# Kernel tuning notes

Hardware: AMD Instinct MI355X
Metric: run time of the kernel (lower is better)

The kernel has to match this reference:

```python
import jax, jax.numpy as jnp
import numpy as np

B, T, C = 1, 4096, 1024
NH, NKV, HD = 16, 4, 64
N_REP = NH // NKV
WIN = 1024
EPS = 1e-5
ROPE_THETA = 10000.0


def setup_inputs() -> dict:
    key = jax.random.key(0)
    ks = jax.random.split(key, 6)
    s = 1.0 / np.sqrt(C)
    x = jax.random.normal(ks[0], (B, T, C), jnp.float32)
    wq = jax.random.normal(ks[1], (NH * HD, C), jnp.float32) * s
    wk = jax.random.normal(ks[2], (NKV * HD, C), jnp.float32) * s
    wv = jax.random.normal(ks[3], (NKV * HD, C), jnp.float32) * s
    wo = jax.random.normal(ks[4], (C, NH * HD), jnp.float32) * (1.0 / np.sqrt(NH * HD))
    q_norm_w = jnp.ones((HD,), jnp.float32)
    k_norm_w = jnp.ones((HD,), jnp.float32)
    # RoPE tables: (T, HD//2)
    inv_freq = 1.0 / (ROPE_THETA ** (np.arange(0, HD, 2, dtype=np.float32) / HD))
    ang = np.outer(np.arange(T, dtype=np.float32), inv_freq)
    freqs_cos = jnp.asarray(np.cos(ang), jnp.float32)
    freqs_sin = jnp.asarray(np.sin(ang), jnp.float32)
    return {"x": x, "wq": wq, "wk": wk, "wv": wv, "wo": wo,
            "q_norm_w": q_norm_w, "k_norm_w": k_norm_w,
            "freqs_cos": freqs_cos, "freqs_sin": freqs_sin}


def _rmsnorm(v, w):
    # RMSNorm over last dim (per-head)
    return v * jax.lax.rsqrt(jnp.mean(v * v, axis=-1, keepdims=True) + EPS) * w


def _rope(v, cos, sin):
    # v: (B, T, H, HD); interleaved complex rotation, matching torch polar freqs_cis
    vr, vi = v[..., 0::2], v[..., 1::2]
    c = cos[None, :, None, :]
    s = sin[None, :, None, :]
    out_r = vr * c - vi * s
    out_i = vr * s + vi * c
    return jnp.stack([out_r, out_i], axis=-1).reshape(v.shape)


def reference(x, wq, wk, wv, wo, q_norm_w, k_norm_w, freqs_cos, freqs_sin):
    xq = jnp.einsum('btc,dc->btd', x, wq).reshape(B, T, NH, HD)
    xk = jnp.einsum('btc,dc->btd', x, wk).reshape(B, T, NKV, HD)
    xv = jnp.einsum('btc,dc->btd', x, wv).reshape(B, T, NKV, HD)
    # per-head QK RMSNorm
    xq = _rmsnorm(xq, q_norm_w)
    xk = _rmsnorm(xk, k_norm_w)
    # RoPE
    xq = _rope(xq, freqs_cos, freqs_sin)
    xk = _rope(xk, freqs_cos, freqs_sin)
    # GQA: expand kv heads
    xk = jnp.repeat(xk, N_REP, axis=2)  # (B, T, NH, HD)
    xv = jnp.repeat(xv, N_REP, axis=2)
    scale = 1.0 / np.sqrt(HD)
    scores = jnp.einsum('bthd,bshd->bhts', xq, xk) * scale
    i = jnp.arange(T)[:, None]
    j = jnp.arange(T)[None, :]
    mask = (i >= j) & (i - j < WIN)  # causal + sliding window
    scores = jnp.where(mask[None, None], scores, -jnp.inf)
    attn = jax.nn.softmax(scores, axis=-1)
    y = jnp.einsum('bhts,bshd->bthd', attn, xv).reshape(B, T, NH * HD)
    return jnp.einsum('btd,cd->btc', y, wo)
```

## Files before the change

kernel.cpp:

```cpp
#include <hip/hip_runtime.h>
#include <hip/hip_bf16.h>


#define WIN_SZ 1024

typedef __attribute__((ext_vector_type(8))) short short8;
typedef __attribute__((ext_vector_type(8))) unsigned short ushort8;
typedef __attribute__((ext_vector_type(4))) float f32x4;
typedef __attribute__((ext_vector_type(16))) float f32x16;

#define GLOAD_LDS16(g, s)                                              \
  __builtin_amdgcn_global_load_lds(                                    \
      (const __attribute__((address_space(1))) unsigned int*)(g),      \
      (__attribute__((address_space(3))) unsigned int*)(s), 16, 0, 0)

__device__ __forceinline__ unsigned short f2bf(float f) {
  union { float f; unsigned u; } v; v.f = f;
  unsigned r = v.u + 0x7fffu + ((v.u >> 16) & 1u);
  return (unsigned short)(r >> 16);
}

__device__ __forceinline__ float bf2f(unsigned short b) {
  union { unsigned u; float f; } v; v.u = ((unsigned)b) << 16; return v.f;
}

__device__ __forceinline__ unsigned pk2bf(float lo, float hi) {
  __hip_bfloat162 h = __float22bfloat162_rn(make_float2(lo, hi));
  union { __hip_bfloat162 h; unsigned u; } c; c.h = h; return c.u;
}

__device__ __forceinline__ short8 frag4(unsigned w0, unsigned w1, unsigned w2, unsigned w3) {
  union { unsigned u[4]; short8 s; } x;
  x.u[0] = w0; x.u[1] = w1; x.u[2] = w2; x.u[3] = w3; return x.s;
}

__global__ __launch_bounds__(256) void k_f2b_all(const float* __restrict__ x,
                                                 const float* __restrict__ wq,
                                                 const float* __restrict__ wk,
                                                 const float* __restrict__ wv,
                                                 const float* __restrict__ wo,
                                                 unsigned short* __restrict__ xb,
                                                 unsigned short* __restrict__ wqkvb,
                                                 unsigned short* __restrict__ wob) {
  int q = blockIdx.x * 256 + threadIdx.x;
  const float* src;
  unsigned short* dst;
  int off;
  if (q < 1048576) { src = x; dst = xb; off = q; }
  else if (q < 1310720) { src = wq; dst = wqkvb; off = q - 1048576; }
  else if (q < 1376256) { src = wk; dst = wqkvb + 1024 * 1024; off = q - 1310720; }
  else if (q < 1441792) { src = wv; dst = wqkvb + 1280 * 1024; off = q - 1376256; }
  else { src = wo; dst = wob; off = q - 1441792; }
  float4 v = ((const float4*)src)[off];
  ushort4 o;
  o.x = f2bf(v.x); o.y = f2bf(v.y); o.z = f2bf(v.z); o.w = f2bf(v.w);
  ((ushort4*)dst)[off] = o;
}

template <int BF16OUT>
__global__ __launch_bounds__(256) void k_gemm2p(const unsigned short* __restrict__ A,
                                                const unsigned short* __restrict__ B,
                                                void* __restrict__ Cv,
                                                int M, int N, int K) {
  __shared__ unsigned short As[2][128 * 64];
  __shared__ unsigned short Bs[2][128 * 64];
  const int tid = threadIdx.x;
  const int w = tid >> 6, l = tid & 63;
  const int wr = w >> 1, wc = w & 1;
  const int r = l & 15, g = l >> 4;
  const int m0 = blockIdx.y * 128, n0 = blockIdx.x * 128;
  const int lr = l >> 3, lc = l & 7;
  const int srowb = w * 32;

  f32x4 acc[4][4];
#pragma unroll
  for (int i = 0; i < 4; i++)
#pragma unroll
    for (int j = 0; j < 4; j++) acc[i][j] = {0.f, 0.f, 0.f, 0.f};

  const unsigned short* Ag = A + (size_t)(m0 + srowb + lr) * K + lc * 8;
  const unsigned short* Bg = B + (size_t)(n0 + srowb + lr) * K + lc * 8;

  auto stage = [&](int buf, int k0) {
#pragma unroll
    for (int it = 0; it < 4; it++) {
      GLOAD_LDS16(Ag + (size_t)(it * 8) * K + k0, &As[buf][(srowb + it * 8) * 64]);
      GLOAD_LDS16(Bg + (size_t)(it * 8) * K + k0, &Bs[buf][(srowb + it * 8) * 64]);
    }
  };

  stage(0, 0);
  __syncthreads();
  int cur = 0;
  const int NT = K >> 6;
  for (int t = 0; t < NT; ++t) {
    if (t + 1 < NT) stage(cur ^ 1, (t + 1) << 6);
    const char* Ab = (const char*)As[cur];
    const char* Bb = (const char*)Bs[cur];
#pragma unroll
    for (int kk = 0; kk < 2; kk++) {
      short8 af[4], bfr[4];
#pragma unroll
      for (int mi = 0; mi < 4; mi++)
        af[mi] = *(const short8*)(Ab + (wr * 64 + mi * 16 + r) * 128 + kk * 64 + g * 16);
#pragma unroll
      for (int nj = 0; nj < 4; nj++)
        bfr[nj] = *(const short8*)(Bb + (wc * 64 + nj * 16 + r) * 128 + kk * 64 + g * 16);
#pragma unroll
      for (int mi = 0; mi < 4; mi++)
#pragma unroll
        for (int nj = 0; nj < 4; nj++)
          acc[mi][nj] = __builtin_amdgcn_mfma_f32_16x16x32_bf16(af[mi], bfr[nj], acc[mi][nj], 0, 0, 0);
    }
    __syncthreads();
    cur ^= 1;
  }

#pragma unroll
  for (int mi = 0; mi < 4; mi++)
#pragma unroll
    for (int nj = 0; nj < 4; nj++) {
      int row = m0 + wr * 64 + mi * 16 + g * 4;
      int col = n0 + wc * 64 + nj * 16 + r;
      if (BF16OUT) {
        unsigned short* C = (unsigned short*)Cv;
#pragma unroll
        for (int e = 0; e < 4; e++)
          C[(size_t)(row + e) * N + col] = f2bf(acc[mi][nj][e]);
      } else {
        float* C = (float*)Cv;
#pragma unroll
        for (int e = 0; e < 4; e++)
          C[(size_t)(row + e) * N + col] = acc[mi][nj][e];
      }
    }
}

__global__ __launch_bounds__(256) void k_normrope(const unsigned short* __restrict__ QKV,
                                                  const float* __restrict__ qw,
                                                  const float* __restrict__ kw,
                                                  const float* __restrict__ fc,
                                                  const float* __restrict__ fs,
                                                  unsigned short* __restrict__ Qb,
                                                  unsigned short* __restrict__ Kb,
                                                  unsigned short* __restrict__ Vtg) {
  int gid = blockIdx.x * 4 + (threadIdx.x >> 6);
  int l = threadIdx.x & 63;
  int t = gid / 24;
  int u = gid - t * 24;
  if (u < 16) {
    float v = bf2f(QKV[(size_t)t * 1536 + u * 64 + l]);
    float ss = v * v;
#pragma unroll
    for (int off = 32; off; off >>= 1) ss += __shfl_xor(ss, off);
    float rms = rsqrtf(ss * (1.0f / 64.0f) + 1e-5f);
    float vn = v * rms * qw[l];
    float c = fc[t * 32 + (l >> 1)], s = fs[t * 32 + (l >> 1)];
    float p = __shfl_xor(vn, 1);
    float out = (l & 1) ? (p * s + vn * c) : (vn * c - p * s);
    Qb[(size_t)t * 1024 + u * 64 + l] = f2bf(out * 0.1803368801111204f);
  } else if (u < 20) {
    int hh = u - 16;
    float v = bf2f(QKV[(size_t)t * 1536 + 1024 + hh * 64 + l]);
    float ss = v * v;
#pragma unroll
    for (int off = 32; off; off >>= 1) ss += __shfl_xor(ss, off);
    float rms = rsqrtf(ss * (1.0f / 64.0f) + 1e-5f);
    float vn = v * rms * kw[l];
    float c = fc[t * 32 + (l >> 1)], s = fs[t * 32 + (l >> 1)];
    float p = __shfl_xor(vn, 1);
    float out = (l & 1) ? (p * s + vn * c) : (vn * c - p * s);
    Kb[(size_t)t * 256 + hh * 64 + l] = f2bf(out);
  } else {
    int hh = u - 20;
    Vtg[(size_t)(hh * 64 + l) * 4096 + t] = QKV[(size_t)t * 1536 + 1280 + hh * 64 + l];
  }
}

__global__ __launch_bounds__(512, 4) void k_attn4(const unsigned short* __restrict__ Qb,
                                                  const unsigned short* __restrict__ Kb,
                                                  const unsigned short* __restrict__ Vtg,
                                                  unsigned short* __restrict__ Yb) {
  __shared__ char smem[4 * 8192 + 1024];
  char* stage = smem;
  float* Obuf = (float*)smem;
  float* ml = (float*)(smem + 32768);

  const int id = blockIdx.x;
  const int cupair = id & 255, sel = id >> 8;
  int qi = cupair >> 1;
  if (sel) qi = 127 - qi;
  const int hk = (cupair & 1) * 2 + sel;
  const int q0 = qi * 32;

  const int tid = threadIdx.x, w = tid >> 6, l = tid & 63;
  const int hh = w & 3, half = w >> 2;
  const int h = hk * 4 + hh;
  const int l31 = l & 31, hi = l >> 5, l15 = l & 15;
  const int qrow = q0 + l31;

  int jlo = q0 - (WIN_SZ - 1);
  if (jlo < 0) jlo = 0;
  jlo &= ~63;
  const int jlast = ((q0 + 31) >> 6) << 6;
  const int nt = ((jlast - jlo) >> 6) + 1;
  const int nh0 = (nt + 1) >> 1;

  const int sb = tid >> 7;
  const int su = tid & 127;
  const int srow = su >> 1;
  const int sg = (su & 1) * 4;
  const int sbase = sb * 8192 + (srow & 31) * 256;
  const int srx = (srow & 15) << 4;
  const int srh = (srow >> 5) * 128;
  const bool isV = sb & 1;
  const unsigned short* gK = Kb + (size_t)srow * 256 + hk * 64 + sg * 8;
  const unsigned short* gV = Vtg + (size_t)(hk * 64 + srow) * 4096 + sg * 8;

  short8 qf[4];
#pragma unroll
  for (int ks = 0; ks < 4; ks++)
    qf[ks] = *(const short8*)(Qb + (size_t)qrow * 1024 + h * 64 + ks * 16 + hi * 8);

  f32x16 accO0, accO1;
#pragma unroll
  for (int i = 0; i < 16; i++) { accO0[i] = 0.f; accO1[i] = 0.f; }
  float m = -1e30f, lsum = 0.f;

  ushort8 pre[4];
  auto prefetch = [&](int s) {
    int jt0 = jlo + (s << 6);
    int t1 = nh0 + s;
    int jt1 = (t1 < nt) ? (jlo + (t1 << 6)) : jlo;
    int jt = (sb >= 2) ? jt1 : jt0;
    if (!isV) {
      const unsigned short* g = gK + (size_t)jt * 256;
#pragma unroll
      for (int e = 0; e < 4; e++) pre[e] = *(const ushort8*)(g + e * 8);
    } else {
      const unsigned short* g = gV + jt;
#pragma unroll
      for (int e = 0; e < 4; e++) pre[e] = *(const ushort8*)(g + e * 8);
    }
  };
  prefetch(0);

  const int kbase = half * 16384;
  const int vbase = kbase + 8192;

  for (int s = 0; s < nh0; ++s) {
    __syncthreads();
#pragma unroll
    for (int e = 0; e < 4; e++) {
      int dst = sbase + ((srh + (sg + e) * 16) ^ srx);
      *(ushort8*)(stage + dst) = pre[e];
    }
    __syncthreads();
    if (s + 1 < nh0) prefetch(s + 1);

    const int myt = half ? (nh0 + s) : s;
    if (myt < nt) {
      const int jt = jlo + (myt << 6);

      f32x16 st0, st1;
#pragma unroll
      for (int i = 0; i < 16; i++) { st0[i] = 0.f; st1[i] = 0.f; }
      __builtin_amdgcn_s_setprio(1);
#pragma unroll
      for (int ks = 0; ks < 4; ks++) {
        int colb = ks * 32 + hi * 16;
        short8 kf0 = *(const short8*)(stage + kbase + l31 * 256 + (colb ^ (l15 << 4)));
        st0 = __builtin_amdgcn_mfma_f32_32x32x16_bf16(kf0, qf[ks], st0, 0, 0, 0);
        short8 kf1 = *(const short8*)(stage + kbase + l31 * 256 + ((128 + colb) ^ (l15 << 4)));
        st1 = __builtin_amdgcn_mfma_f32_32x32x16_bf16(kf1, qf[ks], st1, 0, 0, 0);
      }
      __builtin_amdgcn_s_setprio(0);

      if (jt + 63 > q0 || (q0 + 31) - jt >= WIN_SZ) {
        const int jb = jt + hi * 4;
#pragma unroll
        for (int rg = 0; rg < 16; rg++) {
          int j0 = jb + (rg & 3) + 8 * (rg >> 2);
          if (!((j0 <= qrow) && (qrow - j0 < WIN_SZ))) st0[rg] = -3.0e38f;
          int j1 = j0 + 32;
          if (!((j1 <= qrow) && (qrow - j1 < WIN_SZ))) st1[rg] = -3.0e38f;
        }
      }

      float mx = st0[0];
#pragma unroll
      for (int rg = 1; rg < 16; rg++) mx = fmaxf(mx, st0[rg]);
#pragma unroll
      for (int rg = 0; rg < 16; rg++) mx = fmaxf(mx, st1[rg]);
      mx = fmaxf(mx, __shfl_xor(mx, 32));
      if (!__all(mx <= m + 8.0f)) {
        float mnew = fmaxf(m, mx);
        float alpha = exp2f(m - mnew);
#pragma unroll
        for (int rg = 0; rg < 16; rg++) { accO0[rg] *= alpha; accO1[rg] *= alpha; }
        lsum *= alpha;
        m = mnew;
      }
      float ps = 0.f;
#pragma unroll
      for (int rg = 0; rg < 16; rg++) { st0[rg] = exp2f(st0[rg] - m); ps += st0[rg]; }
#pragma unroll
      for (int rg = 0; rg < 16; rg++) { st1[rg] = exp2f(st1[rg] - m); ps += st1[rg]; }
      lsum += ps;

      unsigned pd0[2][4], pd1[2][4];
#pragma unroll
      for (int b = 0; b < 4; b++) {
        pd0[0][b] = pk2bf(st0[4 * b], st0[4 * b + 1]);
        pd1[0][b] = pk2bf(st0[4 * b + 2], st0[4 * b + 3]);
        pd0[1][b] = pk2bf(st1[4 * b], st1[4 * b + 1]);
        pd1[1][b] = pk2bf(st1[4 * b + 2], st1[4 * b + 3]);
      }

      __builtin_amdgcn_s_setprio(1);
#pragma unroll
      for (int jj = 0; jj < 2; jj++) {
#pragma unroll
        for (int ks2 = 0; ks2 < 2; ks2++) {
          unsigned a0 = pd0[jj][2 * ks2], a1 = pd0[jj][2 * ks2 + 1];
          unsigned b0 = pd1[jj][2 * ks2], b1 = pd1[jj][2 * ks2 + 1];
          unsigned a0x = __shfl_xor(a0, 32), a1x = __shfl_xor(a1, 32);
          unsigned b0x = __shfl_xor(b0, 32), b1x = __shfl_xor(b1, 32);
          unsigned w0 = hi ? a1x : a0;
          unsigned w1 = hi ? b1x : b0;
          unsigned w2 = hi ? a1 : a0x;
          unsigned w3 = hi ? b1 : b0x;
          short8 pf = frag4(w0, w1, w2, w3);
          int colb2 = jj * 64 + ks2 * 32 + hi * 16;
          short8 vf0 = *(const short8*)(stage + vbase + l31 * 256 + (colb2 ^ (l15 << 4)));
          accO0 = __builtin_amdgcn_mfma_f32_32x32x16_bf16(vf0, pf, accO0, 0, 0, 0);
          short8 vf1 = *(const short8*)(stage + vbase + l31 * 256 + ((128 + colb2) ^ (l15 << 4)));
          accO1 = __builtin_amdgcn_mfma_f32_32x32x16_bf16(vf1, pf, accO1, 0, 0, 0);
        }
      }
      __builtin_amdgcn_s_setprio(0);
    }
  }

  lsum += __shfl_xor(lsum, 32);
  __syncthreads();
  if (half == 1) {
#pragma unroll
    for (int dd = 0; dd < 2; dd++) {
      const f32x16& a = dd ? accO1 : accO0;
#pragma unroll
      for (int rg = 0; rg < 16; rg++) {
        int d = dd * 32 + 8 * (rg >> 2) + 4 * hi + (rg & 3);
        Obuf[(hh * 64 + d) * 32 + l31] = a[rg];
      }
    }
    if (!hi) { ml[(hh * 2 + 0) * 32 + l31] = m; ml[(hh * 2 + 1) * 32 + l31] = lsum; }
  }
  __syncthreads();
  if (half == 0) {
    float m1 = ml[(hh * 2 + 0) * 32 + l31];
    float l1 = ml[(hh * 2 + 1) * 32 + l31];
    float ms = fmaxf(m, m1);
    float a0 = exp2f(m - ms), a1 = exp2f(m1 - ms);
    float inv = 1.0f / (lsum * a0 + l1 * a1);
    a0 *= inv; a1 *= inv;
#pragma unroll
    for (int dd = 0; dd < 2; dd++) {
      const f32x16& a = dd ? accO1 : accO0;
#pragma unroll
      for (int b = 0; b < 4; b++) {
        float o[4];
#pragma unroll
        for (int e = 0; e < 4; e++) {
          int d = dd * 32 + 8 * b + 4 * hi + e;
          o[e] = a[4 * b + e] * a0 + Obuf[(hh * 64 + d) * 32 + l31] * a1;
        }
        union { unsigned u[2]; ushort4 v; } ov;
        ov.u[0] = pk2bf(o[0], o[1]);
        ov.u[1] = pk2bf(o[2], o[3]);
        *(ushort4*)(Yb + (size_t)qrow * 1024 + h * 64 + dd * 32 + b * 8 + hi * 4) = ov.v;
      }
    }
  }
}

extern "C" void kernel_launch(void* const* d_in, const int* in_sizes, int n_in,
                              void* d_out, int out_size, void* d_ws, size_t ws_size,
                              hipStream_t stream) {
  const float* x = (const float*)d_in[0];
  const float* wq = (const float*)d_in[1];
  const float* wk = (const float*)d_in[2];
  const float* wv = (const float*)d_in[3];
  const float* wo = (const float*)d_in[4];
  const float* qw = (const float*)d_in[5];
  const float* kw = (const float*)d_in[6];
  const float* fc = (const float*)d_in[7];
  const float* fs = (const float*)d_in[8];
  float* out = (float*)d_out;

  char* p = (char*)d_ws;
  auto alloc = [&](size_t b) {
    char* q = p;
    p += (b + 255) & ~(size_t)255;
    return q;
  };
  unsigned short* xb = (unsigned short*)alloc((size_t)4096 * 1024 * 2);
  unsigned short* wqkvb = (unsigned short*)alloc((size_t)1536 * 1024 * 2);
  unsigned short* wob = (unsigned short*)alloc((size_t)1024 * 1024 * 2);
  unsigned short* QKVb = (unsigned short*)alloc((size_t)4096 * 1536 * 2);
  unsigned short* Qb = (unsigned short*)alloc((size_t)4096 * 1024 * 2);
  unsigned short* Kb = (unsigned short*)alloc((size_t)4096 * 256 * 2);
  unsigned short* Vtg = (unsigned short*)alloc((size_t)256 * 4096 * 2);
  unsigned short* Yb = (unsigned short*)alloc((size_t)4096 * 1024 * 2);

  k_f2b_all<<<6656, 256, 0, stream>>>(x, wq, wk, wv, wo, xb, wqkvb, wob);
  k_gemm2p<1><<<dim3(12, 32), 256, 0, stream>>>(xb, wqkvb, QKVb, 4096, 1536, 1024);
  k_normrope<<<24576, 256, 0, stream>>>(QKVb, qw, kw, fc, fs, Qb, Kb, Vtg);
  k_attn4<<<512, 512, 0, stream>>>(Qb, Kb, Vtg, Yb);
  k_gemm2p<0><<<dim3(8, 32), 256, 0, stream>>>(Yb, wob, out, 4096, 1024, 1024);
}
```

Measured before the change: 123.2 us.

## Use persistent atomic work queue for attention and narrower swizzled GEMM tiles

Attention becomes a persistent kernel of 384 blocks. The blocks pull (query tile, kv head) units from a global atomic counter, ordered longest-first, which should balance the uneven sliding-window workload. The counter is reset by the norm/rope kernel. Both GEMMs switch to 128x64 tiles with a 1D grid and an XCD-aware block swizzle, doubling block count for better CU fill and L2 locality, at the cost of lower arithmetic intensity per block.

```diff
diff --git a/kernel.cpp b/kernel.cpp
--- a/kernel.cpp
+++ b/kernel.cpp
@@ -58,35 +58,41 @@
 }
 
 template <int BF16OUT>
-__global__ __launch_bounds__(256) void k_gemm2p(const unsigned short* __restrict__ A,
-                                                const unsigned short* __restrict__ B,
-                                                void* __restrict__ Cv,
-                                                int M, int N, int K) {
+__global__ __launch_bounds__(256) void k_gemmN64(const unsigned short* __restrict__ A,
+                                                 const unsigned short* __restrict__ B,
+                                                 void* __restrict__ Cv,
+                                                 int M, int N, int K, int nblk) {
   __shared__ unsigned short As[2][128 * 64];
-  __shared__ unsigned short Bs[2][128 * 64];
+  __shared__ unsigned short Bs[2][64 * 64];
+  const int id = blockIdx.x;
+  const int chunk = gridDim.x >> 3;
+  const int swz = (id & 7) * chunk + (id >> 3);
+  const int n_idx = swz % nblk, m_idx = swz / nblk;
+  const int m0 = m_idx * 128, n0 = n_idx * 64;
+
   const int tid = threadIdx.x;
   const int w = tid >> 6, l = tid & 63;
   const int wr = w >> 1, wc = w & 1;
   const int r = l & 15, g = l >> 4;
-  const int m0 = blockIdx.y * 128, n0 = blockIdx.x * 128;
   const int lr = l >> 3, lc = l & 7;
-  const int srowb = w * 32;
-
-  f32x4 acc[4][4];
+  const int srowb = w * 32, browb = w * 16;
+
+  f32x4 acc[4][2];
 #pragma unroll
   for (int i = 0; i < 4; i++)
 #pragma unroll
-    for (int j = 0; j < 4; j++) acc[i][j] = {0.f, 0.f, 0.f, 0.f};
+    for (int j = 0; j < 2; j++) acc[i][j] = {0.f, 0.f, 0.f, 0.f};
 
   const unsigned short* Ag = A + (size_t)(m0 + srowb + lr) * K + lc * 8;
-  const unsigned short* Bg = B + (size_t)(n0 + srowb + lr) * K + lc * 8;
+  const unsigned short* Bg = B + (size_t)(n0 + browb + lr) * K + lc * 8;
 
   auto stage = [&](int buf, int k0) {
 #pragma unroll
-    for (int it = 0; it < 4; it++) {
+    for (int it = 0; it < 4; it++)
       GLOAD_LDS16(Ag + (size_t)(it * 8) * K + k0, &As[buf][(srowb + it * 8) * 64]);
-      GLOAD_LDS16(Bg + (size_t)(it * 8) * K + k0, &Bs[buf][(srowb + it * 8) * 64]);
-    }
+#pragma unroll
+    for (int it = 0; it < 2; it++)
+      GLOAD_LDS16(Bg + (size_t)(it * 8) * K + k0, &Bs[buf][(browb + it * 8) * 64]);
   };
 
   stage(0, 0);
@@ -99,17 +105,17 @@
     const char* Bb = (const char*)Bs[cur];
 #pragma unroll
     for (int kk = 0; kk < 2; kk++) {
-      short8 af[4], bfr[4];
+      short8 af[4], bfr[2];
 #pragma unroll
       for (int mi = 0; mi < 4; mi++)
         af[mi] = *(const short8*)(Ab + (wr * 64 + mi * 16 + r) * 128 + kk * 64 + g * 16);
 #pragma unroll
-      for (int nj = 0; nj < 4; nj++)
-        bfr[nj] = *(const short8*)(Bb + (wc * 64 + nj * 16 + r) * 128 + kk * 64 + g * 16);
+      for (int nj = 0; nj < 2; nj++)
+        bfr[nj] = *(const short8*)(Bb + (wc * 32 + nj * 16 + r) * 128 + kk * 64 + g * 16);
 #pragma unroll
       for (int mi = 0; mi < 4; mi++)
 #pragma unroll
-        for (int nj = 0; nj < 4; nj++)
+        for (int nj = 0; nj < 2; nj++)
           acc[mi][nj] = __builtin_amdgcn_mfma_f32_16x16x32_bf16(af[mi], bfr[nj], acc[mi][nj], 0, 0, 0);
     }
     __syncthreads();
@@ -119,9 +125,9 @@
 #pragma unroll
   for (int mi = 0; mi < 4; mi++)
 #pragma unroll
-    for (int nj = 0; nj < 4; nj++) {
+    for (int nj = 0; nj < 2; nj++) {
       int row = m0 + wr * 64 + mi * 16 + g * 4;
-      int col = n0 + wc * 64 + nj * 16 + r;
+      int col = n0 + wc * 32 + nj * 16 + r;
       if (BF16OUT) {
         unsigned short* C = (unsigned short*)Cv;
 #pragma unroll
@@ -143,7 +149,9 @@
                                                   const float* __restrict__ fs,
                                                   unsigned short* __restrict__ Qb,
                                                   unsigned short* __restrict__ Kb,
-                                                  unsigned short* __restrict__ Vtg) {
+                                                  unsigned short* __restrict__ Vtg,
+                                                  int* __restrict__ ctr) {
+  if (blockIdx.x == 0 && threadIdx.x == 0) *ctr = 0;
   int gid = blockIdx.x * 4 + (threadIdx.x >> 6);
   int l = threadIdx.x & 63;
   int t = gid / 24;
@@ -177,34 +185,20 @@
   }
 }
 
-__global__ __launch_bounds__(512, 4) void k_attn4(const unsigned short* __restrict__ Qb,
+__global__ __launch_bounds__(512, 4) void k_attn5(const unsigned short* __restrict__ Qb,
                                                   const unsigned short* __restrict__ Kb,
                                                   const unsigned short* __restrict__ Vtg,
-                                                  unsigned short* __restrict__ Yb) {
+                                                  unsigned short* __restrict__ Yb,
+                                                  int* __restrict__ ctr) {
   __shared__ char smem[4 * 8192 + 1024];
+  __shared__ int s_unit;
   char* stage = smem;
   float* Obuf = (float*)smem;
   float* ml = (float*)(smem + 32768);
 
-  const int id = blockIdx.x;
-  const int cupair = id & 255, sel = id >> 8;
-  int qi = cupair >> 1;
-  if (sel) qi = 127 - qi;
-  const int hk = (cupair & 1) * 2 + sel;
-  const int q0 = qi * 32;
-
   const int tid = threadIdx.x, w = tid >> 6, l = tid & 63;
   const int hh = w & 3, half = w >> 2;
-  const int h = hk * 4 + hh;
   const int l31 = l & 31, hi = l >> 5, l15 = l & 15;
-  const int qrow = q0 + l31;
-
-  int jlo = q0 - (WIN_SZ - 1);
-  if (jlo < 0) jlo = 0;
-  jlo &= ~63;
-  const int jlast = ((q0 + 31) >> 6) << 6;
-  const int nt = ((jlast - jlo) >> 6) + 1;
-  const int nh0 = (nt + 1) >> 1;
 
   const int sb = tid >> 7;
   const int su = tid & 127;
@@ -214,171 +208,191 @@
   const int srx = (srow & 15) << 4;
   const int srh = (srow >> 5) * 128;
   const bool isV = sb & 1;
-  const unsigned short* gK = Kb + (size_t)srow * 256 + hk * 64 + sg * 8;
-  const unsigned short* gV = Vtg + (size_t)(hk * 64 + srow) * 4096 + sg * 8;
-
-  short8 qf[4];
-#pragma unroll
-  for (int ks = 0; ks < 4; ks++)
-    qf[ks] = *(const short8*)(Qb + (size_t)qrow * 1024 + h * 64 + ks * 16 + hi * 8);
-
-  f32x16 accO0, accO1;
-#pragma unroll
-  for (int i = 0; i < 16; i++) { accO0[i] = 0.f; accO1[i] = 0.f; }
-  float m = -1e30f, lsum = 0.f;
-
-  ushort8 pre[4];
-  auto prefetch = [&](int s) {
-    int jt0 = jlo + (s << 6);
-    int t1 = nh0 + s;
-    int jt1 = (t1 < nt) ? (jlo + (t1 << 6)) : jlo;
-    int jt = (sb >= 2) ? jt1 : jt0;
-    if (!isV) {
-      const unsigned short* g = gK + (size_t)jt * 256;
-#pragma unroll
-      for (int e = 0; e < 4; e++) pre[e] = *(const ushort8*)(g + e * 8);
-    } else {
-      const unsigned short* g = gV + jt;
-#pragma unroll
-      for (int e = 0; e < 4; e++) pre[e] = *(const ushort8*)(g + e * 8);
-    }
-  };
-  prefetch(0);
-
   const int kbase = half * 16384;
   const int vbase = kbase + 8192;
 
-  for (int s = 0; s < nh0; ++s) {
+  for (;;) {
     __syncthreads();
-#pragma unroll
-    for (int e = 0; e < 4; e++) {
-      int dst = sbase + ((srh + (sg + e) * 16) ^ srx);
-      *(ushort8*)(stage + dst) = pre[e];
+    if (tid == 0) s_unit = atomicAdd(ctr, 1);
+    __syncthreads();
+    const int u = s_unit;
+    if (u >= 512) break;
+    const int qi = 127 - (u >> 2);
+    const int hk = u & 3;
+    const int q0 = qi * 32;
+    const int h = hk * 4 + hh;
+    const int qrow = q0 + l31;
+
+    int jlo = q0 - (WIN_SZ - 1);
+    if (jlo < 0) jlo = 0;
+    jlo &= ~63;
+    const int jlast = ((q0 + 31) >> 6) << 6;
+    const int nt = ((jlast - jlo) >> 6) + 1;
+    const int nh0 = (nt + 1) >> 1;
+
+    const unsigned short* gK = Kb + (size_t)srow * 256 + hk * 64 + sg * 8;
+    const unsigned short* gV = Vtg + (size_t)(hk * 64 + srow) * 4096 + sg * 8;
+
+    short8 qf[4];
+#pragma unroll
+    for (int ks = 0; ks < 4; ks++)
+      qf[ks] = *(const short8*)(Qb + (size_t)qrow * 1024 + h * 64 + ks * 16 + hi * 8);
+
+    f32x16 accO0, accO1;
+#pragma unroll
+    for (int i = 0; i < 16; i++) { accO0[i] = 0.f; accO1[i] = 0.f; }
+    float m = -1e30f, lsum = 0.f;
+
+    ushort8 pre[4];
+    auto prefetch = [&](int s) {
+      int jt0 = jlo + (s << 6);
+      int t1 = nh0 + s;
+      int jt1 = (t1 < nt) ? (jlo + (t1 << 6)) : jlo;
+      int jt = (sb >= 2) ? jt1 : jt0;
+      if (!isV) {
+        const unsigned short* g = gK + (size_t)jt * 256;
+#pragma unroll
+        for (int e = 0; e < 4; e++) pre[e] = *(const ushort8*)(g + e * 8);
+      } else {
+        const unsigned short* g = gV + jt;
+#pragma unroll
+        for (int e = 0; e < 4; e++) pre[e] = *(const ushort8*)(g + e * 8);
+      }
+    };
+    prefetch(0);
+
+    for (int s = 0; s < nh0; ++s) {
+      __syncthreads();
+#pragma unroll
+      for (int e = 0; e < 4; e++) {
+        int dst = sbase + ((srh + (sg + e) * 16) ^ srx);
+        *(ushort8*)(stage + dst) = pre[e];
+      }
+      __syncthreads();
+      if (s + 1 < nh0) prefetch(s + 1);
+
+      const int myt = half ? (nh0 + s) : s;
+      if (myt < nt) {
+        const int jt = jlo + (myt << 6);
+
+        f32x16 st0, st1;
+#pragma unroll
+        for (int i = 0; i < 16; i++) { st0[i] = 0.f; st1[i] = 0.f; }
+        __builtin_amdgcn_s_setprio(1);
+#pragma unroll
+        for (int ks = 0; ks < 4; ks++) {
+          int colb = ks * 32 + hi * 16;
+          short8 kf0 = *(const short8*)(stage + kbase + l31 * 256 + (colb ^ (l15 << 4)));
+          st0 = __builtin_amdgcn_mfma_f32_32x32x16_bf16(kf0, qf[ks], st0, 0, 0, 0);
+          short8 kf1 = *(const short8*)(stage + kbase + l31 * 256 + ((128 + colb) ^ (l15 << 4)));
+          st1 = __builtin_amdgcn_mfma_f32_32x32x16_bf16(kf1, qf[ks], st1, 0, 0, 0);
+        }
+        __builtin_amdgcn_s_setprio(0);
+
+        if (jt + 63 > q0 || (q0 + 31) - jt >= WIN_SZ) {
+          const int jb = jt + hi * 4;
+#pragma unroll
+          for (int rg = 0; rg < 16; rg++) {
+            int j0 = jb + (rg & 3) + 8 * (rg >> 2);
+            if (!((j0 <= qrow) && (qrow - j0 < WIN_SZ))) st0[rg] = -3.0e38f;
+            int j1 = j0 + 32;
+            if (!((j1 <= qrow) && (qrow - j1 < WIN_SZ))) st1[rg] = -3.0e38f;
+          }
+        }
+
+        float mx = st0[0];
+#pragma unroll
+        for (int rg = 1; rg < 16; rg++) mx = fmaxf(mx, st0[rg]);
+#pragma unroll
+        for (int rg = 0; rg < 16; rg++) mx = fmaxf(mx, st1[rg]);
+        mx = fmaxf(mx, __shfl_xor(mx, 32));
+        if (!__all(mx <= m + 8.0f)) {
+          float mnew = fmaxf(m, mx);
+          float alpha = exp2f(m - mnew);
+#pragma unroll
+          for (int rg = 0; rg < 16; rg++) { accO0[rg] *= alpha; accO1[rg] *= alpha; }
+          lsum *= alpha;
+          m = mnew;
+        }
+        float ps = 0.f;
+#pragma unroll
+        for (int rg = 0; rg < 16; rg++) { st0[rg] = exp2f(st0[rg] - m); ps += st0[rg]; }
+#pragma unroll
+        for (int rg = 0; rg < 16; rg++) { st1[rg] = exp2f(st1[rg] - m); ps += st1[rg]; }
+        lsum += ps;
+
+        unsigned pd0[2][4], pd1[2][4];
+#pragma unroll
+        for (int b = 0; b < 4; b++) {
+          pd0[0][b] = pk2bf(st0[4 * b], st0[4 * b + 1]);
+          pd1[0][b] = pk2bf(st0[4 * b + 2], st0[4 * b + 3]);
+          pd0[1][b] = pk2bf(st1[4 * b], st1[4 * b + 1]);
+          pd1[1][b] = pk2bf(st1[4 * b + 2], st1[4 * b + 3]);
+        }
+
+        __builtin_amdgcn_s_setprio(1);
+#pragma unroll
+        for (int jj = 0; jj < 2; jj++) {
+#pragma unroll
+          for (int ks2 = 0; ks2 < 2; ks2++) {
+            unsigned a0 = pd0[jj][2 * ks2], a1 = pd0[jj][2 * ks2 + 1];
+            unsigned b0 = pd1[jj][2 * ks2], b1 = pd1[jj][2 * ks2 + 1];
+            unsigned a0x = __shfl_xor(a0, 32), a1x = __shfl_xor(a1, 32);
+            unsigned b0x = __shfl_xor(b0, 32), b1x = __shfl_xor(b1, 32);
+            unsigned w0 = hi ? a1x : a0;
+            unsigned w1 = hi ? b1x : b0;
+            unsigned w2 = hi ? a1 : a0x;
+            unsigned w3 = hi ? b1 : b0x;
+            short8 pf = frag4(w0, w1, w2, w3);
+            int colb2 = jj * 64 + ks2 * 32 + hi * 16;
+            short8 vf0 = *(const short8*)(stage + vbase + l31 * 256 + (colb2 ^ (l15 << 4)));
+            accO0 = __builtin_amdgcn_mfma_f32_32x32x16_bf16(vf0, pf, accO0, 0, 0, 0);
+            short8 vf1 = *(const short8*)(stage + vbase + l31 * 256 + ((128 + colb2) ^ (l15 << 4)));
+            accO1 = __builtin_amdgcn_mfma_f32_32x32x16_bf16(vf1, pf, accO1, 0, 0, 0);
+          }
+        }
+        __builtin_amdgcn_s_setprio(0);
+      }
+    }
+
+    lsum += __shfl_xor(lsum, 32);
+    __syncthreads();
+    if (half == 1) {
+#pragma unroll
+      for (int dd = 0; dd < 2; dd++) {
+        const f32x16& a = dd ? accO1 : accO0;
+#pragma unroll
+        for (int rg = 0; rg < 16; rg++) {
+          int d = dd * 32 + 8 * (rg >> 2) + 4 * hi + (rg & 3);
+          Obuf[(hh * 64 + d) * 32 + l31] = a[rg];
+        }
+      }
+      if (!hi) { ml[(hh * 2 + 0) * 32 + l31] = m; ml[(hh * 2 + 1) * 32 + l31] = lsum; }
     }
     __syncthreads();
-    if (s + 1 < nh0) prefetch(s + 1);
-
-    const int myt = half ? (nh0 + s) : s;
-    if (myt < nt) {
-      const int jt = jlo + (myt << 6);
-
-      f32x16 st0, st1;
-#pragma unroll
-      for (int i = 0; i < 16; i++) { st0[i] = 0.f; st1[i] = 0.f; }
-      __builtin_amdgcn_s_setprio(1);
-#pragma unroll
-      for (int ks = 0; ks < 4; ks++) {
-        int colb = ks * 32 + hi * 16;
-        short8 kf0 = *(const short8*)(stage + kbase + l31 * 256 + (colb ^ (l15 << 4)));
-        st0 = __builtin_amdgcn_mfma_f32_32x32x16_bf16(kf0, qf[ks], st0, 0, 0, 0);
-        short8 kf1 = *(const short8*)(stage + kbase + l31 * 256 + ((128 + colb) ^ (l15 << 4)));
-        st1 = __builtin_amdgcn_mfma_f32_32x32x16_bf16(kf1, qf[ks], st1, 0, 0, 0);
-      }
-      __builtin_amdgcn_s_setprio(0);
-
-      if (jt + 63 > q0 || (q0 + 31) - jt >= WIN_SZ) {
-        const int jb = jt + hi * 4;
-#pragma unroll
-        for (int rg = 0; rg < 16; rg++) {
-          int j0 = jb + (rg & 3) + 8 * (rg >> 2);
-          if (!((j0 <= qrow) && (qrow - j0 < WIN_SZ))) st0[rg] = -3.0e38f;
-          int j1 = j0 + 32;
-          if (!((j1 <= qrow) && (qrow - j1 < WIN_SZ))) st1[rg] = -3.0e38f;
-        }
-      }
-
-      float mx = st0[0];
-#pragma unroll
-      for (int rg = 1; rg < 16; rg++) mx = fmaxf(mx, st0[rg]);
-#pragma unroll
-      for (int rg = 0; rg < 16; rg++) mx = fmaxf(mx, st1[rg]);
-      mx = fmaxf(mx, __shfl_xor(mx, 32));
-      if (!__all(mx <= m + 8.0f)) {
-        float mnew = fmaxf(m, mx);
-        float alpha = exp2f(m - mnew);
-#pragma unroll
-        for (int rg = 0; rg < 16; rg++) { accO0[rg] *= alpha; accO1[rg] *= alpha; }
-        lsum *= alpha;
-        m = mnew;
-      }
-      float ps = 0.f;
-#pragma unroll
-      for (int rg = 0; rg < 16; rg++) { st0[rg] = exp2f(st0[rg] - m); ps += st0[rg]; }
-#pragma unroll
-      for (int rg = 0; rg < 16; rg++) { st1[rg] = exp2f(st1[rg] - m); ps += st1[rg]; }
-      lsum += ps;
-
-      unsigned pd0[2][4], pd1[2][4];
-#pragma unroll
-      for (int b = 0; b < 4; b++) {
-        pd0[0][b] = pk2bf(st0[4 * b], st0[4 * b + 1]);
-        pd1[0][b] = pk2bf(st0[4 * b + 2], st0[4 * b + 3]);
-        pd0[1][b] = pk2bf(st1[4 * b], st1[4 * b + 1]);
-        pd1[1][b] = pk2bf(st1[4 * b + 2], st1[4 * b + 3]);
-      }
-
-      __builtin_amdgcn_s_setprio(1);
-#pragma unroll
-      for (int jj = 0; jj < 2; jj++) {
-#pragma unroll
-        for (int ks2 = 0; ks2 < 2; ks2++) {
-          unsigned a0 = pd0[jj][2 * ks2], a1 = pd0[jj][2 * ks2 + 1];
-          unsigned b0 = pd1[jj][2 * ks2], b1 = pd1[jj][2 * ks2 + 1];
-          unsigned a0x = __shfl_xor(a0, 32), a1x = __shfl_xor(a1, 32);
-          unsigned b0x = __shfl_xor(b0, 32), b1x = __shfl_xor(b1, 32);
-          unsigned w0 = hi ? a1x : a0;
-          unsigned w1 = hi ? b1x : b0;
-          unsigned w2 = hi ? a1 : a0x;
-          unsigned w3 = hi ? b1 : b0x;
-          short8 pf = frag4(w0, w1, w2, w3);
-          int colb2 = jj * 64 + ks2 * 32 + hi * 16;
-          short8 vf0 = *(const short8*)(stage + vbase + l31 * 256 + (colb2 ^ (l15 << 4)));
-          accO0 = __builtin_amdgcn_mfma_f32_32x32x16_bf16(vf0, pf, accO0, 0, 0, 0);
-          short8 vf1 = *(const short8*)(stage + vbase + l31 * 256 + ((128 + colb2) ^ (l15 << 4)));
-          accO1 = __builtin_amdgcn_mfma_f32_32x32x16_bf16(vf1, pf, accO1, 0, 0, 0);
-        }
-      }
-      __builtin_amdgcn_s_setprio(0);
-    }
-  }
-
-  lsum += __shfl_xor(lsum, 32);
-  __syncthreads();
-  if (half == 1) {
-#pragma unroll
-    for (int dd = 0; dd < 2; dd++) {
-      const f32x16& a = dd ? accO1 : accO0;
-#pragma unroll
-      for (int rg = 0; rg < 16; rg++) {
-        int d = dd * 32 + 8 * (rg >> 2) + 4 * hi + (rg & 3);
-        Obuf[(hh * 64 + d) * 32 + l31] = a[rg];
-      }
-    }
-    if (!hi) { ml[(hh * 2 + 0) * 32 + l31] = m; ml[(hh * 2 + 1) * 32 + l31] = lsum; }
-  }
-  __syncthreads();
-  if (half == 0) {
-    float m1 = ml[(hh * 2 + 0) * 32 + l31];
-    float l1 = ml[(hh * 2 + 1) * 32 + l31];
-    float ms = fmaxf(m, m1);
-    float a0 = exp2f(m - ms), a1 = exp2f(m1 - ms);
-    float inv = 1.0f / (lsum * a0 + l1 * a1);
-    a0 *= inv; a1 *= inv;
-#pragma unroll
-    for (int dd = 0; dd < 2; dd++) {
-      const f32x16& a = dd ? accO1 : accO0;
-#pragma unroll
-      for (int b = 0; b < 4; b++) {
-        float o[4];
-#pragma unroll
-        for (int e = 0; e < 4; e++) {
-          int d = dd * 32 + 8 * b + 4 * hi + e;
-          o[e] = a[4 * b + e] * a0 + Obuf[(hh * 64 + d) * 32 + l31] * a1;
-        }
-        union { unsigned u[2]; ushort4 v; } ov;
-        ov.u[0] = pk2bf(o[0], o[1]);
-        ov.u[1] = pk2bf(o[2], o[3]);
-        *(ushort4*)(Yb + (size_t)qrow * 1024 + h * 64 + dd * 32 + b * 8 + hi * 4) = ov.v;
+    if (half == 0) {
+      float m1 = ml[(hh * 2 + 0) * 32 + l31];
+      float l1 = ml[(hh * 2 + 1) * 32 + l31];
+      float ms = fmaxf(m, m1);
+      float a0 = exp2f(m - ms), a1 = exp2f(m1 - ms);
+      float inv = 1.0f / (lsum * a0 + l1 * a1);
+      a0 *= inv; a1 *= inv;
+#pragma unroll
+      for (int dd = 0; dd < 2; dd++) {
+        const f32x16& a = dd ? accO1 : accO0;
+#pragma unroll
+        for (int b = 0; b < 4; b++) {
+          float o[4];
+#pragma unroll
+          for (int e = 0; e < 4; e++) {
+            int d = dd * 32 + 8 * b + 4 * hi + e;
+            o[e] = a[4 * b + e] * a0 + Obuf[(hh * 64 + d) * 32 + l31] * a1;
+          }
+          union { unsigned uu[2]; ushort4 v; } ov;
+          ov.uu[0] = pk2bf(o[0], o[1]);
+          ov.uu[1] = pk2bf(o[2], o[3]);
+          *(ushort4*)(Yb + (size_t)qrow * 1024 + h * 64 + dd * 32 + b * 8 + hi * 4) = ov.v;
+        }
       }
     }
   }
@@ -412,10 +426,11 @@
   unsigned short* Kb = (unsigned short*)alloc((size_t)4096 * 256 * 2);
   unsigned short* Vtg = (unsigned short*)alloc((size_t)256 * 4096 * 2);
   unsigned short* Yb = (unsigned short*)alloc((size_t)4096 * 1024 * 2);
+  int* ctr = (int*)alloc(256);
 
   k_f2b_all<<<6656, 256, 0, stream>>>(x, wq, wk, wv, wo, xb, wqkvb, wob);
-  k_gemm2p<1><<<dim3(12, 32), 256, 0, stream>>>(xb, wqkvb, QKVb, 4096, 1536, 1024);
-  k_normrope<<<24576, 256, 0, stream>>>(QKVb, qw, kw, fc, fs, Qb, Kb, Vtg);
-  k_attn4<<<512, 512, 0, stream>>>(Qb, Kb, Vtg, Yb);
-  k_gemm2p<0><<<dim3(8, 32), 256, 0, stream>>>(Yb, wob, out, 4096, 1024, 1024);
-}
+  k_gemmN64<1><<<768, 256, 0, stream>>>(xb, wqkvb, QKVb, 4096, 1536, 1024, 24);
+  k_normrope<<<24576, 256, 0, stream>>>(QKVb, qw, kw, fc, fs, Qb, Kb, Vtg, ctr);
+  k_attn5<<<384, 512, 0, stream>>>(Qb, Kb, Vtg, Yb, ctr);
+  k_gemmN64<0><<<512, 256, 0, stream>>>(Yb, wob, out, 4096, 1024, 1024, 16);
+}
```

Result: slower. 135.0 us (+9.6%).
